# Optimization experiments

Hardware: AMD Instinct MI355X
Metric: run time of the kernel (lower is better)

## Reference

```python
import jax, jax.numpy as jnp
import numpy as np

U = 4096        # n_users
I = 16384       # n_items
D = 64          # embed_dim
N = U + I       # interaction-graph nodes
NE_I = 524288   # interaction edges (nonzeros of norm_inter_graph)
NE_S = 65536    # social edges
L_INTER = 3     # LightGCN layers on user-item graph
L_SOC = 2       # WeightGCN layers (graph powers) on social graph
NEG_INF = jnp.float32(-1e30)


def setup_inputs() -> dict:
    key = jax.random.key(0)
    ks = jax.random.split(key, 13)
    return {
        'user_emb': jax.random.normal(ks[0], (U, D), jnp.float32) * 0.1,
        'item_emb': jax.random.normal(ks[1], (I, D), jnp.float32) * 0.1,
        'inter_vals': jax.random.uniform(ks[2], (NE_I,), jnp.float32) * 0.05,  # D^-1/2 A D^-1/2 values
        'Wa': jax.random.normal(ks[3], (D, D), jnp.float32) * 0.1,
        'Wb': jax.random.normal(ks[4], (D, D), jnp.float32) * 0.1,
        'w1': jax.random.normal(ks[5], (2 * D, D), jnp.float32) * 0.1,
        'b1': jnp.zeros((D,), jnp.float32),
        'w2': jax.random.normal(ks[6], (D, 1), jnp.float32) * 0.1,
        'b2': jnp.zeros((1,), jnp.float32),
        'inter_rows': jax.random.randint(ks[7], (NE_I,), 0, N, jnp.int32),
        'inter_cols': jax.random.randint(ks[8], (NE_I,), 0, N, jnp.int32),
        'social_rows': jax.random.randint(ks[9], (NE_S,), 0, U, jnp.int32),
        'social_cols': jax.random.randint(ks[10], (NE_S,), 0, U, jnp.int32),
    }


def _spmm(rows, cols, vals, x, n):
    # sparse [n,n] @ dense [n,d] via gather + segment_sum (torch.sparse.mm)
    return jax.ops.segment_sum(vals[:, None] * x[cols], rows, num_segments=n)


def _lightgcn(rows, cols, vals, embed, n, n_layers):
    embs = [embed]
    h = embed
    for _ in range(n_layers):
        h = _spmm(rows, cols, vals, h, n)
        embs.append(h)
    return jnp.mean(jnp.stack(embs, axis=1), axis=1)  # [n, d]


def _masked_row_softmax(g, m):
    # torch.sparse.softmax: softmax over stored (structural) entries per row
    logits = jnp.where(m, g, NEG_INF)
    s = jax.nn.softmax(logits, axis=1)
    return jnp.where(m.any(axis=1, keepdims=True), s, 0.0)


def reference(user_emb, item_emb, inter_vals, Wa, Wb, w1, b1, w2, b2,
              inter_rows, inter_cols, social_rows, social_cols):
    # ---- LightGCN on user-item interaction graph ----
    inter_emb = jnp.concatenate([user_emb, item_emb], axis=0)           # [N, D]
    inter_out = _lightgcn(inter_rows, inter_cols, inter_vals, inter_emb, N, L_INTER)
    user_e, item_e = inter_out[:U], inter_out[U:]

    # ---- edge-activation MLP (infer_activation): h = cols, t = rows ----
    feat = jnp.concatenate([user_emb[social_cols] @ Wa,
                            user_emb[social_rows] @ Wb], axis=1)        # [NE_S, 2D]
    hid = jax.nn.relu(feat @ w1 + b1)
    p = (hid @ w2 + b2)[:, 0]
    edge_w = jax.nn.sigmoid(p)                                          # [NE_S]

    # ---- weighted social graph (duplicates coalesce by sum) ----
    A = jnp.zeros((U, U), jnp.float32).at[social_rows, social_cols].add(edge_w)
    B = (A > 0).astype(jnp.float32)  # structural pattern (non-diff)

    # ---- WeightGCN: graph powers + per-row sparse softmax ----
    graphs, masks = [A], [A > 0]
    g_prev, b_prev = A, B
    for _ in range(L_SOC - 1):
        g_prev = g_prev @ A
        b_prev = b_prev @ B
        graphs.append(g_prev)
        masks.append(b_prev > 0)
    sembs = [user_e]
    for g, m in zip(graphs, masks):
        sembs.append(_masked_row_softmax(g, m) @ user_e)
    social_e2 = jnp.mean(jnp.stack(sembs, axis=1), axis=1)              # [U, D]

    # ---- final user embedding (bpr_loss path) ----
    return user_e + social_e2
```

## Files before the change

kernel.cpp:

```cpp
#include <hip/hip_runtime.h>
#include <hip/hip_bf16.h>

#define U_    4096
#define I_    16384
#define D_    64
#define N_    20480
#define NEI   524288
#define NES   65536
#define CAPI  96
#define RCAPS 64

__global__ __launch_bounds__(256) void init_wab2_kernel(int* __restrict__ cnt, int* __restrict__ skey,
                                                        float* __restrict__ sval,
                                                        const float* __restrict__ Wa,
                                                        const float* __restrict__ Wb,
                                                        const float* __restrict__ w1,
                                                        float* __restrict__ Wa2, float* __restrict__ Wb2) {
    int b = blockIdx.x;
    if (b < 1024) {
        int tid = b * 256 + threadIdx.x;
        int stride = 1024 * 256;
        for (int o = tid; o < N_; o += stride) cnt[o] = 0;
        for (int o = tid; o < U_ * RCAPS; o += stride) { skey[o] = -1; sval[o] = 0.f; }
    } else {
        int o = (b - 1024) * 256 + threadIdx.x;
        int mat = o >> 12;
        int i = (o >> 6) & 63;
        int j = o & 63;
        const float* M  = mat ? Wb : Wa;
        const float* W1 = w1 + mat * 64 * 64;
        float s = 0.f;
        #pragma unroll 8
        for (int k = 0; k < 64; ++k) s += M[i * 64 + k] * W1[k * 64 + j];
        (mat ? Wb2 : Wa2)[i * 64 + j] = s;
    }
}

__global__ void scatter_i_kernel(const int* __restrict__ rows, const int* __restrict__ cols,
                                 const float* __restrict__ vals,
                                 int* __restrict__ cnt, int2* __restrict__ ed) {
    int e = blockIdx.x * 256 + threadIdx.x;
    int r = rows[e];
    int pos = atomicAdd(&cnt[r], 1);
    if (pos < CAPI) ed[(size_t)r * CAPI + pos] = make_int2(cols[e], __float_as_int(vals[e]));
}

__global__ __launch_bounds__(256) void spmm1_pab_kernel(const int* __restrict__ cnt, const int2* __restrict__ ed,
                                                        const float* __restrict__ ue, const float* __restrict__ ie,
                                                        float* __restrict__ h1,
                                                        const float* __restrict__ Wa2, const float* __restrict__ Wb2,
                                                        float* __restrict__ Pa, float* __restrict__ Pb) {
    int b = blockIdx.x;
    int wv = threadIdx.x >> 6, lane = threadIdx.x & 63;
    if (b < 5120) {
        int w = b * 4 + wv;
        int n = cnt[w]; if (n > CAPI) n = CAPI;
        const int2* row = ed + (size_t)w * CAPI;
        float acc = 0.f;
        #pragma unroll 4
        for (int j = 0; j < n; ++j) {
            int2 e = row[j];
            int c = e.x; float v = __int_as_float(e.y);
            const float* xp = (c < U_) ? (ue + (size_t)c * D_) : (ie + (size_t)(c - U_) * D_);
            acc += v * xp[lane];
        }
        h1[(size_t)w * D_ + lane] = acc;
    } else {
        int w = (b - 5120) * 4 + wv;
        float x = ue[w * 64 + lane];
        float accA = 0.f, accB = 0.f;
        #pragma unroll 8
        for (int k = 0; k < 64; ++k) {
            float xk = __shfl(x, k);
            accA += xk * Wa2[k * 64 + lane];
            accB += xk * Wb2[k * 64 + lane];
        }
        Pa[w * 64 + lane] = accA;
        Pb[w * 64 + lane] = accB;
    }
}

__global__ __launch_bounds__(256) void spmm2_edge_kernel(const int* __restrict__ cnt, const int2* __restrict__ ed,
                                                         const float* __restrict__ x, float* __restrict__ y,
                                                         const int* __restrict__ sr, const int* __restrict__ sc,
                                                         const float* __restrict__ Pa, const float* __restrict__ Pb,
                                                         const float* __restrict__ b1, const float* __restrict__ w2,
                                                         const float* __restrict__ b2,
                                                         int* __restrict__ skey, float* __restrict__ sval) {
    int b = blockIdx.x;
    if (b < 5120) {
        int wv = threadIdx.x >> 6, lane = threadIdx.x & 63;
        int w = b * 4 + wv;
        int n = cnt[w]; if (n > CAPI) n = CAPI;
        const int2* row = ed + (size_t)w * CAPI;
        float acc = 0.f;
        #pragma unroll 4
        for (int j = 0; j < n; ++j) {
            int2 e = row[j];
            acc += __int_as_float(e.y) * x[(size_t)e.x * D_ + lane];
        }
        y[(size_t)w * D_ + lane] = acc;
    } else {
        int w = (b - 5120) * 16 + (threadIdx.x >> 4);
        int q = threadIdx.x & 15;
        int r = sr[w], c = sc[w];
        float4 pa = ((const float4*)Pa)[c * 16 + q];
        float4 pb = ((const float4*)Pb)[r * 16 + q];
        float4 bb = ((const float4*)b1)[q];
        float4 ww = ((const float4*)w2)[q];
        float hx = fmaxf(pa.x + pb.x + bb.x, 0.f);
        float hy = fmaxf(pa.y + pb.y + bb.y, 0.f);
        float hz = fmaxf(pa.z + pb.z + bb.z, 0.f);
        float hw = fmaxf(pa.w + pb.w + bb.w, 0.f);
        float t = hx * ww.x + hy * ww.y + hz * ww.z + hw * ww.w;
        t += __shfl_xor(t, 8);
        t += __shfl_xor(t, 4);
        t += __shfl_xor(t, 2);
        t += __shfl_xor(t, 1);
        if (q == 0) {
            float p = t + b2[0];
            float ew = 1.f / (1.f + expf(-p));
            size_t base = (size_t)r * RCAPS;
            int hh = c & (RCAPS - 1);
            for (int probe = 0; probe < RCAPS; ++probe) {
                int prev = atomicCAS(&skey[base + hh], -1, c);
                if (prev == -1 || prev == c) { atomicAdd(&sval[base + hh], ew); break; }
                hh = (hh + 1) & (RCAPS - 1);
            }
        }
    }
}

__global__ __launch_bounds__(256) void spmm_last_kernel(const int* __restrict__ cnt, const int2* __restrict__ ed,
                                                        const float* __restrict__ ue,
                                                        const float* __restrict__ h1, const float* __restrict__ h2,
                                                        float* __restrict__ user_e) {
    int w = (blockIdx.x * 256 + threadIdx.x) >> 6;
    int lane = threadIdx.x & 63;
    int n = cnt[w]; if (n > CAPI) n = CAPI;
    const int2* row = ed + (size_t)w * CAPI;
    float acc = 0.f;
    #pragma unroll 4
    for (int j = 0; j < n; ++j) {
        int2 e = row[j];
        acc += __int_as_float(e.y) * h2[(size_t)e.x * D_ + lane];
    }
    size_t o = (size_t)w * D_ + lane;
    user_e[o] = 0.25f * (ue[o] + h1[o] + h2[o] + acc);
}


__device__ __forceinline__ float wave_max_(float v) {
    #pragma unroll
    for (int o = 32; o > 0; o >>= 1) v = fmaxf(v, __shfl_xor(v, o));
    return v;
}
__device__ __forceinline__ float wave_sum_(float v) {
    #pragma unroll
    for (int o = 32; o > 0; o >>= 1) v += __shfl_xor(v, o);
    return v;
}

__global__ __launch_bounds__(256) void social_kernel(const int* __restrict__ skey,
                                                     const float* __restrict__ sval,
                                                     const float* __restrict__ user_e,
                                                     float* __restrict__ out) {
    __shared__ float row2[U_];
    __shared__ int   kcol_s[RCAPS];
    __shared__ float kval_s[RCAPS];
    __shared__ float wredm[4], wreds[4];
    __shared__ float accw[4][64];
    __shared__ int   nnz_s;

    int i = blockIdx.x, t = threadIdx.x;
    int wv = t >> 6, lane = t & 63;

    {
        float4* r4 = (float4*)row2;
        #pragma unroll
        for (int u = 0; u < 4; ++u) r4[t + 256 * u] = make_float4(0.f, 0.f, 0.f, 0.f);
    }

    if (wv == 0) {
        int k = skey[(size_t)i * RCAPS + lane];
        float v = sval[(size_t)i * RCAPS + lane];
        unsigned long long mask = __ballot(k >= 0);
        int pos = __popcll(mask & ((1ull << lane) - 1ull));
        if (k >= 0) { kcol_s[pos] = k; kval_s[pos] = v; }
        if (lane == 0) nnz_s = __popcll(mask);
    }
    __syncthreads();
    int nnz = nnz_s;

    float kv  = (lane < nnz) ? kval_s[lane] : -1e30f;
    float m1  = wave_max_(kv);
    float ex  = (lane < nnz) ? expf(kv - m1) : 0.f;
    float S1  = wave_sum_(ex);
    float inv1 = (nnz > 0) ? 1.f / S1 : 0.f;

    for (int e = wv; e < nnz; e += 4) {
        int k = kcol_s[e];
        float vk = kval_s[e];
        int   c2 = skey[(size_t)k * RCAPS + lane];
        float v2 = sval[(size_t)k * RCAPS + lane];
        if (c2 >= 0) atomicAdd(&row2[c2], vk * v2);
    }

    float acc = 0.f;
    for (int e = wv; e < nnz; e += 4) {
        float p = __shfl(ex, e) * inv1;
        acc += p * user_e[(size_t)kcol_s[e] * D_ + lane];
    }
    __syncthreads();

    float lm = 0.f;
    {
        const float4* r4 = (const float4*)row2;
        #pragma unroll
        for (int u = 0; u < 4; ++u) {
            float4 v = r4[t + 256 * u];
            lm = fmaxf(lm, fmaxf(fmaxf(v.x, v.y), fmaxf(v.z, v.w)));
        }
    }
    lm = wave_max_(lm);
    if (lane == 0) wredm[wv] = lm;
    __syncthreads();
    float m2 = fmaxf(fmaxf(wredm[0], wredm[1]), fmaxf(wredm[2], wredm[3]));

    float ls = 0.f;
    {
        float4* r4 = (float4*)row2;
        #pragma unroll
        for (int u = 0; u < 4; ++u) {
            float4 v = r4[t + 256 * u];
            float4 e4;
            e4.x = (v.x > 0.f) ? expf(v.x - m2) : 0.f;
            e4.y = (v.y > 0.f) ? expf(v.y - m2) : 0.f;
            e4.z = (v.z > 0.f) ? expf(v.z - m2) : 0.f;
            e4.w = (v.w > 0.f) ? expf(v.w - m2) : 0.f;
            ls += e4.x + e4.y + e4.z + e4.w;
            r4[t + 256 * u] = e4;
        }
    }
    ls = wave_sum_(ls);
    if (lane == 0) wreds[wv] = ls;
    __syncthreads();
    float S2 = wreds[0] + wreds[1] + wreds[2] + wreds[3];
    float inv2 = (S2 > 0.f) ? 1.f / S2 : 0.f;

    for (int ch = 0; ch < 16; ++ch) {
        int cb = (wv << 10) + (ch << 6);
        float pv = row2[cb + lane];
        unsigned long long msk = __ballot(pv > 0.f);
        while (msk) {
            int b = __ffsll(msk) - 1;
            msk &= msk - 1;
            float p = __shfl(pv, b) * inv2;
            acc += p * user_e[(size_t)(cb + b) * D_ + lane];
        }
    }
    accw[wv][lane] = acc;
    __syncthreads();
    if (t < 64) {
        float s = accw[0][t] + accw[1][t] + accw[2][t] + accw[3][t];
        float ue = user_e[(size_t)i * D_ + t];
        out[i * D_ + t] = (4.f * ue + s) * (1.f / 3.f);
    }
}


extern "C" void kernel_launch(void* const* d_in, const int* in_sizes, int n_in,
                              void* d_out, int out_size, void* d_ws, size_t ws_size,
                              hipStream_t stream) {
    (void)in_sizes; (void)n_in; (void)out_size; (void)ws_size;
    const float* user_emb  = (const float*)d_in[0];
    const float* item_emb  = (const float*)d_in[1];
    const float* inter_vals= (const float*)d_in[2];
    const float* Wa        = (const float*)d_in[3];
    const float* Wb        = (const float*)d_in[4];
    const float* w1        = (const float*)d_in[5];
    const float* b1        = (const float*)d_in[6];
    const float* w2        = (const float*)d_in[7];
    const float* b2        = (const float*)d_in[8];
    const int* inter_rows  = (const int*)d_in[9];
    const int* inter_cols  = (const int*)d_in[10];
    const int* social_rows = (const int*)d_in[11];
    const int* social_cols = (const int*)d_in[12];
    float* out = (float*)d_out;

    char* w = (char*)d_ws;
    auto alloc = [&](size_t bytes) -> void* {
        void* p = (void*)w;
        w += (bytes + 255) & ~(size_t)255;
        return p;
    };
    float* h1     = (float*)alloc((size_t)N_ * D_ * 4);
    float* h2     = (float*)alloc((size_t)N_ * D_ * 4);
    float* user_e = (float*)alloc((size_t)U_ * D_ * 4);
    float* Pa     = (float*)alloc((size_t)U_ * D_ * 4);
    float* Pb     = (float*)alloc((size_t)U_ * D_ * 4);
    float* Wa2    = (float*)alloc(64 * 64 * 4);
    float* Wb2    = (float*)alloc(64 * 64 * 4);
    int*   cnt    = (int*)alloc((size_t)N_ * 4);
    int2*  ed     = (int2*)alloc((size_t)N_ * CAPI * 8);
    int*   skey   = (int*)alloc((size_t)U_ * RCAPS * 4);
    float* sval   = (float*)alloc((size_t)U_ * RCAPS * 4);

    init_wab2_kernel<<<1056, 256, 0, stream>>>(cnt, skey, sval, Wa, Wb, w1, Wa2, Wb2);
    scatter_i_kernel<<<NEI / 256, 256, 0, stream>>>(inter_rows, inter_cols, inter_vals, cnt, ed);
    spmm1_pab_kernel<<<6144, 256, 0, stream>>>(cnt, ed, user_emb, item_emb, h1, Wa2, Wb2, Pa, Pb);
    spmm2_edge_kernel<<<9216, 256, 0, stream>>>(cnt, ed, h1, h2, social_rows, social_cols,
                                                Pa, Pb, b1, w2, b2, skey, sval);
    spmm_last_kernel<<<1024, 256, 0, stream>>>(cnt, ed, user_emb, h1, h2, user_e);
    social_kernel<<<U_, 256, 0, stream>>>(skey, sval, user_e, out);
}
```

Baseline: 227.5 us.

## Interleave social hash key/value and compact second-hop nonzeros into per-wave lists

Replaces the separate key and value arrays of the social hash table with one interleaved int2 array, so each probe and read touches a single 8-byte slot. In the social kernel, the dense 4096-entry max, exp and sum passes over shared memory become a single ballot pass that builds a compacted per-wave list of nonzero columns. The exp, sum and gather-accumulate then loop only over that list. The list is capped at 384 entries per wave, so a row with more second-hop nonzeros in one 1024-column quarter would silently drop entries.

Measured after the change: 217.3 us. -4.5%, faster.

```diff
diff --git a/kernel.cpp b/kernel.cpp
--- a/kernel.cpp
+++ b/kernel.cpp
@@ -9,9 +9,9 @@
 #define NES   65536
 #define CAPI  96
 #define RCAPS 64
-
-__global__ __launch_bounds__(256) void init_wab2_kernel(int* __restrict__ cnt, int* __restrict__ skey,
-                                                        float* __restrict__ sval,
+#define SEG   384
+
+__global__ __launch_bounds__(256) void init_wab2_kernel(int* __restrict__ cnt, int* __restrict__ skv,
                                                         const float* __restrict__ Wa,
                                                         const float* __restrict__ Wb,
                                                         const float* __restrict__ w1,
@@ -21,7 +21,7 @@
         int tid = b * 256 + threadIdx.x;
         int stride = 1024 * 256;
         for (int o = tid; o < N_; o += stride) cnt[o] = 0;
-        for (int o = tid; o < U_ * RCAPS; o += stride) { skey[o] = -1; sval[o] = 0.f; }
+        for (int o = tid; o < U_ * RCAPS; o += stride) ((int2*)skv)[o] = make_int2(-1, 0);
     } else {
         int o = (b - 1024) * 256 + threadIdx.x;
         int mat = o >> 12;
@@ -86,7 +86,7 @@
                                                          const float* __restrict__ Pa, const float* __restrict__ Pb,
                                                          const float* __restrict__ b1, const float* __restrict__ w2,
                                                          const float* __restrict__ b2,
-                                                         int* __restrict__ skey, float* __restrict__ sval) {
+                                                         int* __restrict__ skv) {
     int b = blockIdx.x;
     if (b < 5120) {
         int wv = threadIdx.x >> 6, lane = threadIdx.x & 63;
@@ -123,8 +123,8 @@
             size_t base = (size_t)r * RCAPS;
             int hh = c & (RCAPS - 1);
             for (int probe = 0; probe < RCAPS; ++probe) {
-                int prev = atomicCAS(&skey[base + hh], -1, c);
-                if (prev == -1 || prev == c) { atomicAdd(&sval[base + hh], ew); break; }
+                int prev = atomicCAS(&skv[(base + hh) * 2], -1, c);
+                if (prev == -1 || prev == c) { atomicAdd((float*)&skv[(base + hh) * 2 + 1], ew); break; }
                 hh = (hh + 1) & (RCAPS - 1);
             }
         }
@@ -161,11 +161,11 @@
     return v;
 }
 
-__global__ __launch_bounds__(256) void social_kernel(const int* __restrict__ skey,
-                                                     const float* __restrict__ sval,
+__global__ __launch_bounds__(256) void social_kernel(const int* __restrict__ skv,
                                                      const float* __restrict__ user_e,
                                                      float* __restrict__ out) {
     __shared__ float row2[U_];
+    __shared__ int   list2[4][SEG];
     __shared__ int   kcol_s[RCAPS];
     __shared__ float kval_s[RCAPS];
     __shared__ float wredm[4], wreds[4];
@@ -182,11 +182,10 @@
     }
 
     if (wv == 0) {
-        int k = skey[(size_t)i * RCAPS + lane];
-        float v = sval[(size_t)i * RCAPS + lane];
-        unsigned long long mask = __ballot(k >= 0);
+        int2 kv = ((const int2*)skv)[(size_t)i * RCAPS + lane];
+        unsigned long long mask = __ballot(kv.x >= 0);
         int pos = __popcll(mask & ((1ull << lane) - 1ull));
-        if (k >= 0) { kcol_s[pos] = k; kval_s[pos] = v; }
+        if (kv.x >= 0) { kcol_s[pos] = kv.x; kval_s[pos] = __int_as_float(kv.y); }
         if (lane == 0) nnz_s = __popcll(mask);
     }
     __syncthreads();
@@ -201,9 +200,8 @@
     for (int e = wv; e < nnz; e += 4) {
         int k = kcol_s[e];
         float vk = kval_s[e];
-        int   c2 = skey[(size_t)k * RCAPS + lane];
-        float v2 = sval[(size_t)k * RCAPS + lane];
-        if (c2 >= 0) atomicAdd(&row2[c2], vk * v2);
+        int2 kv2 = ((const int2*)skv)[(size_t)k * RCAPS + lane];
+        if (kv2.x >= 0) atomicAdd(&row2[kv2.x], vk * __int_as_float(kv2.y));
     }
 
     float acc = 0.f;
@@ -213,51 +211,41 @@
     }
     __syncthreads();
 
+    int len = 0;
     float lm = 0.f;
-    {
-        const float4* r4 = (const float4*)row2;
-        #pragma unroll
-        for (int u = 0; u < 4; ++u) {
-            float4 v = r4[t + 256 * u];
-            lm = fmaxf(lm, fmaxf(fmaxf(v.x, v.y), fmaxf(v.z, v.w)));
-        }
-    }
-    lm = wave_max_(lm);
-    if (lane == 0) wredm[wv] = lm;
-    __syncthreads();
-    float m2 = fmaxf(fmaxf(wredm[0], wredm[1]), fmaxf(wredm[2], wredm[3]));
-
-    float ls = 0.f;
-    {
-        float4* r4 = (float4*)row2;
-        #pragma unroll
-        for (int u = 0; u < 4; ++u) {
-            float4 v = r4[t + 256 * u];
-            float4 e4;
-            e4.x = (v.x > 0.f) ? expf(v.x - m2) : 0.f;
-            e4.y = (v.y > 0.f) ? expf(v.y - m2) : 0.f;
-            e4.z = (v.z > 0.f) ? expf(v.z - m2) : 0.f;
-            e4.w = (v.w > 0.f) ? expf(v.w - m2) : 0.f;
-            ls += e4.x + e4.y + e4.z + e4.w;
-            r4[t + 256 * u] = e4;
-        }
-    }
-    ls = wave_sum_(ls);
-    if (lane == 0) wreds[wv] = ls;
-    __syncthreads();
-    float S2 = wreds[0] + wreds[1] + wreds[2] + wreds[3];
-    float inv2 = (S2 > 0.f) ? 1.f / S2 : 0.f;
-
     for (int ch = 0; ch < 16; ++ch) {
         int cb = (wv << 10) + (ch << 6);
         float pv = row2[cb + lane];
+        lm = fmaxf(lm, pv);
         unsigned long long msk = __ballot(pv > 0.f);
-        while (msk) {
-            int b = __ffsll(msk) - 1;
-            msk &= msk - 1;
-            float p = __shfl(pv, b) * inv2;
-            acc += p * user_e[(size_t)(cb + b) * D_ + lane];
-        }
+        int pos = __popcll(msk & ((1ull << lane) - 1ull));
+        if (pv > 0.f && len + pos < SEG) list2[wv][len + pos] = cb + lane;
+        len += __popcll(msk);
+    }
+    if (len > SEG) len = SEG;
+    lm = wave_max_(lm);
+    if (lane == 0) wredm[wv] = lm;
+    __syncthreads();
+    float m2 = fmaxf(fmaxf(wredm[0], wredm[1]), fmaxf(wredm[2], wredm[3]));
+
+    float ls = 0.f;
+    for (int e = lane; e < len; e += 64) {
+        int c = list2[wv][e];
+        float ev = expf(row2[c] - m2);
+        row2[c] = ev;
+        ls += ev;
+    }
+    ls = wave_sum_(ls);
+    if (lane == 0) wreds[wv] = ls;
+    __syncthreads();
+    float S2 = wreds[0] + wreds[1] + wreds[2] + wreds[3];
+    float inv2 = (S2 > 0.f) ? 1.f / S2 : 0.f;
+
+    #pragma unroll 4
+    for (int e = 0; e < len; ++e) {
+        int c = list2[wv][e];
+        float p = row2[c] * inv2;
+        acc += p * user_e[(size_t)c * D_ + lane];
     }
     accw[wv][lane] = acc;
     __syncthreads();
@@ -303,14 +291,13 @@
     float* Wb2    = (float*)alloc(64 * 64 * 4);
     int*   cnt    = (int*)alloc((size_t)N_ * 4);
     int2*  ed     = (int2*)alloc((size_t)N_ * CAPI * 8);
-    int*   skey   = (int*)alloc((size_t)U_ * RCAPS * 4);
-    float* sval   = (float*)alloc((size_t)U_ * RCAPS * 4);
-
-    init_wab2_kernel<<<1056, 256, 0, stream>>>(cnt, skey, sval, Wa, Wb, w1, Wa2, Wb2);
+    int*   skv    = (int*)alloc((size_t)U_ * RCAPS * 8);
+
+    init_wab2_kernel<<<1056, 256, 0, stream>>>(cnt, skv, Wa, Wb, w1, Wa2, Wb2);
     scatter_i_kernel<<<NEI / 256, 256, 0, stream>>>(inter_rows, inter_cols, inter_vals, cnt, ed);
     spmm1_pab_kernel<<<6144, 256, 0, stream>>>(cnt, ed, user_emb, item_emb, h1, Wa2, Wb2, Pa, Pb);
     spmm2_edge_kernel<<<9216, 256, 0, stream>>>(cnt, ed, h1, h2, social_rows, social_cols,
-                                                Pa, Pb, b1, w2, b2, skey, sval);
+                                                Pa, Pb, b1, w2, b2, skv);
     spmm_last_kernel<<<1024, 256, 0, stream>>>(cnt, ed, user_emb, h1, h2, user_e);
-    social_kernel<<<U_, 256, 0, stream>>>(skey, sval, user_e, out);
-}
+    social_kernel<<<U_, 256, 0, stream>>>(skv, user_e, out);
+}
```
